# Performance work log

Hardware: AMD Instinct MI355X
Metric: run time of the kernel (lower is better)

Reference implementation:

```python
import jax, jax.numpy as jnp
import numpy as np


def setup_inputs() -> dict:
    key = jax.random.key(0)
    k1, k2, k3 = jax.random.split(key, 3)
    B, Cin, H, W = 16, 128, 56, 56
    Cout, Kh, Kw = 256, 3, 3
    tensor = jax.random.normal(k1, (B, Cin, H, W), dtype=jnp.float32)
    weights = jax.random.normal(k2, (Cout, Cin, Kh, Kw), dtype=jnp.float32) * 0.05
    bias = jax.random.normal(k3, (Cout,), dtype=jnp.float32) * 0.05
    return {"tensor": tensor, "weights": weights, "bias": bias}


def reference(tensor, weights, bias):
    # OpticalConvolution: unfold (im2col) -> per-output-channel augmented dot
    # products (w . patch + b). Mathematically this is a standard 2D conv with
    # bias, expressed here as one fused conv instead of a per-channel loop.
    stride, padding, dilation = (1, 1), ((1, 1), (1, 1)), (1, 1)
    out = jax.lax.conv_general_dilated(
        tensor, weights,
        window_strides=stride,
        padding=padding,
        rhs_dilation=dilation,
        dimension_numbers=("NCHW", "OIHW", "NCHW"),
    )
    return out + bias[None, :, None, None]  # [B, Cout, H_out, W_out]
```

## Files before the change

### kernel.cpp

```cpp
#include <hip/hip_runtime.h>
#include <hip/hip_bf16.h>

typedef unsigned short ushort_t;
typedef unsigned int uint_t;

#define CIN   128
#define COUT  256
#define HH    56
#define WW    56
#define HWSZ  3136
#define BATCH 16
#define NPIX  50176
#define KTOT  1152

typedef __attribute__((ext_vector_type(8))) short bf16x8;
typedef __attribute__((ext_vector_type(4))) float f32x4;

__device__ __forceinline__ ushort_t f2bf(float v) {
    union { float f; uint_t u; } c; c.f = v;
    uint_t u = c.u;
    u += 0x7FFFu + ((u >> 16) & 1u);
    return (ushort_t)(u >> 16);
}

__device__ __forceinline__ uint_t pk2bf(float lo, float hi) {
    __hip_bfloat162 h = __float22bfloat162_rn(make_float2(lo, hi));
    union { __hip_bfloat162 h; uint_t u; } c; c.h = h;
    return c.u;
}

__global__ __launch_bounds__(256) void prep(
    const float* __restrict__ tensor, const float* __restrict__ weights,
    ushort_t* __restrict__ Ib, ushort_t* __restrict__ A2, ushort_t* __restrict__ guard)
{
    __shared__ __align__(16) uint_t lds_u[64 * 68];
    const int tid = threadIdx.x;

    if (blockIdx.x < 784) {
        int t   = blockIdx.x;
        int b   = t / 49;
        int hwt = t - b * 49;
        int hw0 = hwt * 64;
        const float* src = tensor + (size_t)b * CIN * HWSZ + hw0;
        #pragma unroll
        for (int k = 0; k < 4; ++k) {
            int t2 = tid + k * 256;
            int hb = t2 & 15;
            int cp = t2 >> 4;
            const float* s0 = src + (size_t)(2 * cp) * HWSZ + hb * 4;
            float4 a  = *(const float4*)s0;
            float4 bb = *(const float4*)(s0 + HWSZ);
            uint_t w0 = pk2bf(a.x, bb.x);
            uint_t w1 = pk2bf(a.y, bb.y);
            uint_t w2 = pk2bf(a.z, bb.z);
            uint_t w3 = pk2bf(a.w, bb.w);
            int c16  = cp >> 2;
            int lb   = cp & 3;
            int c16p = c16 ^ (hb & 7);
            uint_t* base = &lds_u[(hb * 4) * 68 + c16p * 4 + lb];
            base[0 * 68] = w0;
            base[1 * 68] = w1;
            base[2 * 68] = w2;
            base[3 * 68] = w3;
        }
        __syncthreads();
        ushort_t* dst = Ib + ((size_t)b * HWSZ + hw0) * CIN;
        #pragma unroll
        for (int k = 0; k < 4; ++k) {
            int s2  = tid + k * 256;
            int ho  = s2 >> 4;
            int c16 = s2 & 15;
            int c16p = c16 ^ ((ho >> 2) & 7);
            uint4 v = *(const uint4*)&lds_u[ho * 68 + c16p * 4];
            *(uint4*)(dst + ho * 128 + c16 * 8) = v;
        }
    } else {
        int co = blockIdx.x - 784;
        ushort_t* lds_s = (ushort_t*)lds_u;
        const float* src = weights + (size_t)co * KTOT;
        #pragma unroll
        for (int k = 0; k < 5; ++k) {
            int idx = tid + k * 256;
            if (idx < KTOT) {
                int ci  = idx / 9;
                int pos = idx - ci * 9;
                lds_s[pos * 128 + ci] = f2bf(src[idx]);
            }
        }
        __syncthreads();
        int mt  = co >> 6;
        int ii  = (co >> 4) & 3;
        int l16 = co & 15;
        if (tid < 144) {
            int s    = tid >> 2;
            int quad = tid & 3;
            uint4 v = *(const uint4*)&lds_s[(s >> 2) * 128 + (s & 3) * 32 + quad * 8];
            *(uint4*)(A2 + ((size_t)((mt * 36 + s) * 4 + ii) * 64 + quad * 16 + l16) * 8) = v;
        }
        if (blockIdx.x == 784 && tid < 128) ((uint_t*)guard)[tid] = 0;
    }
}

__global__ __launch_bounds__(128, 3) void conv_gemm(
    const ushort_t* __restrict__ A2,
    const ushort_t* __restrict__ Ib,
    const float* __restrict__ bias,
    float* __restrict__ out,
    const ushort_t* __restrict__ guard)
{
    __shared__ ushort_t B_lds[2][64 * 32];

    const int tid  = threadIdx.x;
    const int wave = tid >> 6;
    const int lane = tid & 63;
    const int quad = lane >> 4;
    const int l16  = lane & 15;

    const int g  = blockIdx.x >> 4;
    const int bm = (blockIdx.x >> 3) & 1;
    const int bn = g * 8 + (blockIdx.x & 7);
    const int mt = bm * 2 + wave;

    int bOff[9][2];
    #pragma unroll
    for (int k = 0; k < 2; ++k) {
        int slot = k * 128 + tid;
        int r  = slot >> 2;
        int c  = slot & 3;
        int cF = c ^ ((r >> 1) & 3);
        int pix = bn * 64 + r;
        int b_  = pix / HWSZ;
        int rem = pix - b_ * HWSZ;
        int y_  = rem / WW;
        int x_  = rem - y_ * WW;
        int base = pix * CIN + cF * 8;
        int goff = (int)(guard - Ib);
        #pragma unroll
        for (int pos = 0; pos < 9; ++pos) {
            const int dy = pos / 3 - 1;
            const int dx = pos % 3 - 1;
            int yy = y_ + dy, xx = x_ + dx;
            bool ok = ((uint_t)yy < (uint_t)HH) && ((uint_t)xx < (uint_t)WW);
            bOff[pos][k] = ok ? (base + (dy * WW + dx) * CIN) : goff;
        }
    }
    const int xorc = (l16 >> 1) & 3;

    const ushort_t* aBase = A2 + ((size_t)mt * 36 * 4 * 64 + lane) * 8;

    auto stageB = [&](int s, int buf) {
        const int pos = s >> 2;
        const int cc  = s & 3;
        #pragma unroll
        for (int k = 0; k < 2; ++k) {
            __builtin_amdgcn_global_load_lds(
                (const __attribute__((address_space(1))) void*)(Ib + bOff[pos][k] + cc * 32),
                (__attribute__((address_space(3))) void*)(&B_lds[buf][(k * 128 + wave * 64) * 8]),
                16, 0, 0);
        }
    };

    const f32x4 zero = {0.f, 0.f, 0.f, 0.f};
    f32x4 acc[4][4];
    #pragma unroll
    for (int i = 0; i < 4; ++i)
        #pragma unroll
        for (int j = 0; j < 4; ++j) acc[i][j] = zero;

    bf16x8 aCur[4], aNxt[4];
    stageB(0, 0);
    #pragma unroll
    for (int i = 0; i < 4; ++i)
        aCur[i] = *(const bf16x8*)(aBase + (size_t)i * 512);

    #pragma unroll
    for (int s = 0; s < 36; ++s) {
        __syncthreads();
        if (s < 35) {
            stageB(s + 1, (s + 1) & 1);
            #pragma unroll
            for (int i = 0; i < 4; ++i)
                aNxt[i] = *(const bf16x8*)(aBase + (size_t)((s + 1) * 4 + i) * 512);
        }
        const int p = s & 1;
        bf16x8 bfr[4];
        #pragma unroll
        for (int j = 0; j < 4; ++j)
            bfr[j] = *(const bf16x8*)&B_lds[p][(j * 16 + l16) * 32 + (quad ^ xorc) * 8];
        #pragma unroll
        for (int i = 0; i < 4; ++i)
            #pragma unroll
            for (int j = 0; j < 4; ++j)
                acc[i][j] = __builtin_amdgcn_mfma_f32_16x16x32_bf16(
                    aCur[i], bfr[j], acc[i][j], 0, 0, 0);
        #pragma unroll
        for (int i = 0; i < 4; ++i) aCur[i] = aNxt[i];
    }

    int obase[4];
    #pragma unroll
    for (int j = 0; j < 4; ++j) {
        int pix = bn * 64 + j * 16 + l16;
        int b_  = pix / HWSZ;
        int rem = pix - b_ * HWSZ;
        obase[j] = b_ * (COUT * HWSZ) + rem;
    }
    #pragma unroll
    for (int i = 0; i < 4; ++i) {
        #pragma unroll
        for (int r = 0; r < 4; ++r) {
            int co = bm * 128 + wave * 64 + i * 16 + quad * 4 + r;
            float bv = bias[co];
            int coOff = co * HWSZ;
            #pragma unroll
            for (int j = 0; j < 4; ++j) {
                out[(size_t)(obase[j] + coOff)] = acc[i][j][r] + bv;
            }
        }
    }
}

__global__ void naive_conv(const float* __restrict__ in, const float* __restrict__ w,
                           const float* __restrict__ bias, float* __restrict__ out, int total) {
    int idx = blockIdx.x * 256 + threadIdx.x;
    if (idx >= total) return;
    int x = idx % WW; int t = idx / WW;
    int y = t % HH; t /= HH;
    int co = t % COUT; int b = t / COUT;
    float s = bias[co];
    const float* wr = w + (size_t)co * KTOT;
    for (int ci = 0; ci < CIN; ++ci) {
        const float* ir = in + (size_t)(b * CIN + ci) * HWSZ;
        for (int kh = 0; kh < 3; ++kh) {
            int yy = y + kh - 1;
            if ((uint_t)yy >= (uint_t)HH) continue;
            for (int kw = 0; kw < 3; ++kw) {
                int xx = x + kw - 1;
                if ((uint_t)xx >= (uint_t)WW) continue;
                s += ir[yy * WW + xx] * wr[ci * 9 + kh * 3 + kw];
            }
        }
    }
    out[idx] = s;
}

extern "C" void kernel_launch(void* const* d_in, const int* in_sizes, int n_in,
                              void* d_out, int out_size, void* d_ws, size_t ws_size,
                              hipStream_t stream) {
    const float* tensor  = (const float*)d_in[0];
    const float* weights = (const float*)d_in[1];
    const float* bias    = (const float*)d_in[2];
    float* out = (float*)d_out;

    const size_t GUARD    = 1024;
    const size_t A2_BYTES = (size_t)COUT * KTOT * 2;
    const size_t IB_BYTES = (size_t)NPIX * CIN * 2;
    const size_t NEED     = GUARD + A2_BYTES + IB_BYTES;

    if (ws_size >= NEED) {
        ushort_t* guard = (ushort_t*)d_ws;
        ushort_t* A2    = (ushort_t*)((char*)d_ws + GUARD);
        ushort_t* Ib    = (ushort_t*)((char*)d_ws + GUARD + A2_BYTES);
        prep<<<784 + COUT, 256, 0, stream>>>(tensor, weights, Ib, A2, guard);
        conv_gemm<<<2 * 784, 128, 0, stream>>>(A2, Ib, bias, out, guard);
    } else {
        int total = BATCH * COUT * HWSZ;
        naive_conv<<<(total + 255) / 256, 256, 0, stream>>>(tensor, weights, bias, out, total);
    }
}
```

Baseline: 129.9 us.

## Fuse input transpose into conv via LDS halo patch, drop im2col buffer

Replaces the separate NCHW-to-NHWC bf16 prep pass and the guarded global im2col gathers with a conv kernel in which each block loads a zero-padded 4-row halo patch of the input (all 128 channels) straight from fp32 into LDS. Each 256-thread block now computes all 256 output channels for 112 pixels (two image rows), with the 9 filter taps read as shifted windows of that patch. This removes the intermediate Ib write and read and a full pass over the input, and reuses each input row across taps. In exchange the block uses about 63 KB of LDS and 28 accumulators per lane, which limits occupancy, and the main loop no longer double-buffers B through LDS.

```diff
diff --git a/kernel.cpp b/kernel.cpp
--- a/kernel.cpp
+++ b/kernel.cpp
@@ -13,6 +13,9 @@
 #define NPIX  50176
 #define KTOT  1152
 
+#define PROW_U 68
+#define PATCH_U (4 * 58 * 68)
+
 typedef __attribute__((ext_vector_type(8))) short bf16x8;
 typedef __attribute__((ext_vector_type(4))) float f32x4;
 
@@ -29,193 +32,149 @@
     return c.u;
 }
 
-__global__ __launch_bounds__(256) void prep(
-    const float* __restrict__ tensor, const float* __restrict__ weights,
-    ushort_t* __restrict__ Ib, ushort_t* __restrict__ A2, ushort_t* __restrict__ guard)
+__global__ __launch_bounds__(256) void wprep(
+    const float* __restrict__ weights, ushort_t* __restrict__ A2)
 {
-    __shared__ __align__(16) uint_t lds_u[64 * 68];
+    __shared__ ushort_t lds_s[KTOT];
     const int tid = threadIdx.x;
-
-    if (blockIdx.x < 784) {
-        int t   = blockIdx.x;
-        int b   = t / 49;
-        int hwt = t - b * 49;
-        int hw0 = hwt * 64;
-        const float* src = tensor + (size_t)b * CIN * HWSZ + hw0;
-        #pragma unroll
-        for (int k = 0; k < 4; ++k) {
-            int t2 = tid + k * 256;
-            int hb = t2 & 15;
-            int cp = t2 >> 4;
-            const float* s0 = src + (size_t)(2 * cp) * HWSZ + hb * 4;
-            float4 a  = *(const float4*)s0;
-            float4 bb = *(const float4*)(s0 + HWSZ);
-            uint_t w0 = pk2bf(a.x, bb.x);
-            uint_t w1 = pk2bf(a.y, bb.y);
-            uint_t w2 = pk2bf(a.z, bb.z);
-            uint_t w3 = pk2bf(a.w, bb.w);
-            int c16  = cp >> 2;
-            int lb   = cp & 3;
-            int c16p = c16 ^ (hb & 7);
-            uint_t* base = &lds_u[(hb * 4) * 68 + c16p * 4 + lb];
-            base[0 * 68] = w0;
-            base[1 * 68] = w1;
-            base[2 * 68] = w2;
-            base[3 * 68] = w3;
-        }
-        __syncthreads();
-        ushort_t* dst = Ib + ((size_t)b * HWSZ + hw0) * CIN;
-        #pragma unroll
-        for (int k = 0; k < 4; ++k) {
-            int s2  = tid + k * 256;
-            int ho  = s2 >> 4;
-            int c16 = s2 & 15;
-            int c16p = c16 ^ ((ho >> 2) & 7);
-            uint4 v = *(const uint4*)&lds_u[ho * 68 + c16p * 4];
-            *(uint4*)(dst + ho * 128 + c16 * 8) = v;
-        }
-    } else {
-        int co = blockIdx.x - 784;
-        ushort_t* lds_s = (ushort_t*)lds_u;
-        const float* src = weights + (size_t)co * KTOT;
-        #pragma unroll
-        for (int k = 0; k < 5; ++k) {
-            int idx = tid + k * 256;
-            if (idx < KTOT) {
-                int ci  = idx / 9;
-                int pos = idx - ci * 9;
-                lds_s[pos * 128 + ci] = f2bf(src[idx]);
-            }
-        }
-        __syncthreads();
-        int mt  = co >> 6;
-        int ii  = (co >> 4) & 3;
-        int l16 = co & 15;
-        if (tid < 144) {
-            int s    = tid >> 2;
-            int quad = tid & 3;
-            uint4 v = *(const uint4*)&lds_s[(s >> 2) * 128 + (s & 3) * 32 + quad * 8];
-            *(uint4*)(A2 + ((size_t)((mt * 36 + s) * 4 + ii) * 64 + quad * 16 + l16) * 8) = v;
-        }
-        if (blockIdx.x == 784 && tid < 128) ((uint_t*)guard)[tid] = 0;
-    }
-}
-
-__global__ __launch_bounds__(128, 3) void conv_gemm(
+    const int co  = blockIdx.x;
+    const float* src = weights + (size_t)co * KTOT;
+    #pragma unroll
+    for (int k = 0; k < 5; ++k) {
+        int idx = tid + k * 256;
+        if (idx < KTOT) {
+            int ci  = idx / 9;
+            int pos = idx - ci * 9;
+            lds_s[pos * 128 + ci] = f2bf(src[idx]);
+        }
+    }
+    __syncthreads();
+    int mt  = co >> 6;
+    int ii  = (co >> 4) & 3;
+    int l16 = co & 15;
+    if (tid < 144) {
+        int s    = tid >> 2;
+        int quad = tid & 3;
+        uint4 v = *(const uint4*)&lds_s[(s >> 2) * 128 + (s & 3) * 32 + quad * 8];
+        *(uint4*)(A2 + ((size_t)((mt * 36 + s) * 4 + ii) * 64 + quad * 16 + l16) * 8) = v;
+    }
+}
+
+__global__ __launch_bounds__(256, 2) void conv_direct(
     const ushort_t* __restrict__ A2,
-    const ushort_t* __restrict__ Ib,
+    const float* __restrict__ tensor,
     const float* __restrict__ bias,
-    float* __restrict__ out,
-    const ushort_t* __restrict__ guard)
+    float* __restrict__ out)
 {
-    __shared__ ushort_t B_lds[2][64 * 32];
-
+    __shared__ __align__(16) uint_t patch[PATCH_U];
     const int tid  = threadIdx.x;
     const int wave = tid >> 6;
     const int lane = tid & 63;
     const int quad = lane >> 4;
     const int l16  = lane & 15;
 
-    const int g  = blockIdx.x >> 4;
-    const int bm = (blockIdx.x >> 3) & 1;
-    const int bn = g * 8 + (blockIdx.x & 7);
-    const int mt = bm * 2 + wave;
-
-    int bOff[9][2];
-    #pragma unroll
-    for (int k = 0; k < 2; ++k) {
-        int slot = k * 128 + tid;
-        int r  = slot >> 2;
-        int c  = slot & 3;
-        int cF = c ^ ((r >> 1) & 3);
-        int pix = bn * 64 + r;
-        int b_  = pix / HWSZ;
-        int rem = pix - b_ * HWSZ;
-        int y_  = rem / WW;
-        int x_  = rem - y_ * WW;
-        int base = pix * CIN + cF * 8;
-        int goff = (int)(guard - Ib);
-        #pragma unroll
-        for (int pos = 0; pos < 9; ++pos) {
-            const int dy = pos / 3 - 1;
-            const int dx = pos % 3 - 1;
-            int yy = y_ + dy, xx = x_ + dx;
-            bool ok = ((uint_t)yy < (uint_t)HH) && ((uint_t)xx < (uint_t)WW);
-            bOff[pos][k] = ok ? (base + (dy * WW + dx) * CIN) : goff;
-        }
-    }
-    const int xorc = (l16 >> 1) & 3;
-
-    const ushort_t* aBase = A2 + ((size_t)mt * 36 * 4 * 64 + lane) * 8;
-
-    auto stageB = [&](int s, int buf) {
-        const int pos = s >> 2;
-        const int cc  = s & 3;
-        #pragma unroll
-        for (int k = 0; k < 2; ++k) {
-            __builtin_amdgcn_global_load_lds(
-                (const __attribute__((address_space(1))) void*)(Ib + bOff[pos][k] + cc * 32),
-                (__attribute__((address_space(3))) void*)(&B_lds[buf][(k * 128 + wave * 64) * 8]),
-                16, 0, 0);
-        }
-    };
+    const int bn = blockIdx.x;
+    const int b  = bn / 28;
+    const int y0 = (bn - b * 28) * 2;
+
+    #pragma unroll
+    for (int k = 0; k < 16; ++k) {
+        int i4 = tid + k * 256;
+        if (i4 < PATCH_U / 4) *(uint4*)&patch[i4 * 4] = make_uint4(0u, 0u, 0u, 0u);
+    }
+    __syncthreads();
+
+    const float* src_b = tensor + (size_t)b * CIN * HWSZ;
+    #pragma unroll
+    for (int it = 0; it < 16; ++it) {
+        int xq = tid & 15;
+        int t2 = it * 16 + (tid >> 4);
+        int cp = t2 & 63;
+        int pr = t2 >> 6;
+        int y  = y0 - 1 + pr;
+        if (xq < 14 && (uint_t)y < (uint_t)HH) {
+            const float* s0 = src_b + (size_t)(2 * cp) * HWSZ + y * WW + xq * 4;
+            float4 va = *(const float4*)s0;
+            float4 vb = *(const float4*)(s0 + HWSZ);
+            uint_t* dst = &patch[(pr * 58 + xq * 4 + 1) * PROW_U + cp];
+            dst[0 * PROW_U] = pk2bf(va.x, vb.x);
+            dst[1 * PROW_U] = pk2bf(va.y, vb.y);
+            dst[2 * PROW_U] = pk2bf(va.z, vb.z);
+            dst[3 * PROW_U] = pk2bf(va.w, vb.w);
+        }
+    }
+    __syncthreads();
+
+    const ushort_t* patch_s = (const ushort_t*)patch;
+    int bbase[7];
+    #pragma unroll
+    for (int j = 0; j < 7; ++j) {
+        int p  = j * 16 + l16;
+        int ro = p / 56;
+        int x  = p - ro * 56;
+        bbase[j] = (ro * 58 + x) * 136 + quad * 8;
+    }
+
+    const ushort_t* aPtr = A2 + ((size_t)(wave * 144) * 64 + lane) * 8;
+    bf16x8 aCur[4], aNxt[4];
+    #pragma unroll
+    for (int i = 0; i < 4; ++i) aCur[i] = *(const bf16x8*)(aPtr + i * 512);
 
     const f32x4 zero = {0.f, 0.f, 0.f, 0.f};
-    f32x4 acc[4][4];
+    f32x4 acc[4][7];
     #pragma unroll
     for (int i = 0; i < 4; ++i)
         #pragma unroll
-        for (int j = 0; j < 4; ++j) acc[i][j] = zero;
-
-    bf16x8 aCur[4], aNxt[4];
-    stageB(0, 0);
-    #pragma unroll
-    for (int i = 0; i < 4; ++i)
-        aCur[i] = *(const bf16x8*)(aBase + (size_t)i * 512);
-
-    #pragma unroll
-    for (int s = 0; s < 36; ++s) {
-        __syncthreads();
-        if (s < 35) {
-            stageB(s + 1, (s + 1) & 1);
+        for (int j = 0; j < 7; ++j) acc[i][j] = zero;
+
+    #pragma unroll
+    for (int pos = 0; pos < 9; ++pos) {
+        const int dy = pos / 3 - 1;
+        const int dx = pos % 3 - 1;
+        const int poff = ((dy + 1) * 58 + (dx + 1)) * 136;
+        #pragma unroll
+        for (int cc = 0; cc < 4; ++cc) {
+            const int s = pos * 4 + cc;
+            if (s < 35) {
+                aPtr += 2048;
+                #pragma unroll
+                for (int i = 0; i < 4; ++i)
+                    aNxt[i] = *(const bf16x8*)(aPtr + i * 512);
+            }
+            bf16x8 bfr[7];
+            #pragma unroll
+            for (int j = 0; j < 7; ++j)
+                bfr[j] = *(const bf16x8*)&patch_s[bbase[j] + poff + cc * 32];
             #pragma unroll
             for (int i = 0; i < 4; ++i)
-                aNxt[i] = *(const bf16x8*)(aBase + (size_t)((s + 1) * 4 + i) * 512);
-        }
-        const int p = s & 1;
-        bf16x8 bfr[4];
-        #pragma unroll
-        for (int j = 0; j < 4; ++j)
-            bfr[j] = *(const bf16x8*)&B_lds[p][(j * 16 + l16) * 32 + (quad ^ xorc) * 8];
-        #pragma unroll
-        for (int i = 0; i < 4; ++i)
-            #pragma unroll
-            for (int j = 0; j < 4; ++j)
-                acc[i][j] = __builtin_amdgcn_mfma_f32_16x16x32_bf16(
-                    aCur[i], bfr[j], acc[i][j], 0, 0, 0);
-        #pragma unroll
-        for (int i = 0; i < 4; ++i) aCur[i] = aNxt[i];
-    }
-
-    int obase[4];
-    #pragma unroll
-    for (int j = 0; j < 4; ++j) {
-        int pix = bn * 64 + j * 16 + l16;
-        int b_  = pix / HWSZ;
-        int rem = pix - b_ * HWSZ;
-        obase[j] = b_ * (COUT * HWSZ) + rem;
-    }
+                #pragma unroll
+                for (int j = 0; j < 7; ++j)
+                    acc[i][j] = __builtin_amdgcn_mfma_f32_16x16x32_bf16(
+                        aCur[i], bfr[j], acc[i][j], 0, 0, 0);
+            #pragma unroll
+            for (int i = 0; i < 4; ++i) aCur[i] = aNxt[i];
+        }
+    }
+
+    int opix[7];
+    #pragma unroll
+    for (int j = 0; j < 7; ++j) {
+        int p  = j * 16 + l16;
+        int ro = p / 56;
+        int x  = p - ro * 56;
+        opix[j] = (y0 + ro) * WW + x;
+    }
+    const size_t bout = (size_t)b * (COUT * HWSZ);
     #pragma unroll
     for (int i = 0; i < 4; ++i) {
         #pragma unroll
         for (int r = 0; r < 4; ++r) {
-            int co = bm * 128 + wave * 64 + i * 16 + quad * 4 + r;
+            int co = wave * 64 + i * 16 + quad * 4 + r;
             float bv = bias[co];
-            int coOff = co * HWSZ;
-            #pragma unroll
-            for (int j = 0; j < 4; ++j) {
-                out[(size_t)(obase[j] + coOff)] = acc[i][j][r] + bv;
-            }
+            size_t obase = bout + (size_t)co * HWSZ;
+            #pragma unroll
+            for (int j = 0; j < 7; ++j)
+                out[obase + opix[j]] = acc[i][j][r] + bv;
         }
     }
 }
@@ -252,17 +211,12 @@
     const float* bias    = (const float*)d_in[2];
     float* out = (float*)d_out;
 
-    const size_t GUARD    = 1024;
     const size_t A2_BYTES = (size_t)COUT * KTOT * 2;
-    const size_t IB_BYTES = (size_t)NPIX * CIN * 2;
-    const size_t NEED     = GUARD + A2_BYTES + IB_BYTES;
-
-    if (ws_size >= NEED) {
-        ushort_t* guard = (ushort_t*)d_ws;
-        ushort_t* A2    = (ushort_t*)((char*)d_ws + GUARD);
-        ushort_t* Ib    = (ushort_t*)((char*)d_ws + GUARD + A2_BYTES);
-        prep<<<784 + COUT, 256, 0, stream>>>(tensor, weights, Ib, A2, guard);
-        conv_gemm<<<2 * 784, 128, 0, stream>>>(A2, Ib, bias, out, guard);
+
+    if (ws_size >= A2_BYTES) {
+        ushort_t* A2 = (ushort_t*)d_ws;
+        wprep<<<COUT, 256, 0, stream>>>(weights, A2);
+        conv_direct<<<NPIX / 112, 256, 0, stream>>>(A2, tensor, bias, out);
     } else {
         int total = BATCH * COUT * HWSZ;
         naive_conv<<<(total + 255) / 256, 256, 0, stream>>>(tensor, weights, bias, out, total);
```

Result: faster. 110.3 us (-15.1%).
